# Performance work log

Measured on AMD Instinct MI355X. Metric: run time of the kernel, lower is better.

Reference implementation:

```python
import jax, jax.numpy as jnp
import numpy as np
from jax.scipy.linalg import expm

DIM = 1024
N_ROT = 3


def setup_inputs() -> dict:
    key = jax.random.key(0)
    k1, k2 = jax.random.split(key)
    x = jax.random.normal(k1, (4, 4096, DIM), dtype=jnp.float32)
    # raw parameter tensors; skew-symmetrization (as in reset_parameters) done in reference
    generators = jax.random.normal(k2, (N_ROT, DIM, DIM), dtype=jnp.float32) * 0.02
    return {"x": x, "generators": generators}


def reference(x, generators):
    # skew-symmetrize each generator: G <- 0.5*(G - G^T)
    gens = 0.5 * (generators - jnp.swapaxes(generators, -1, -2))
    # sequential rotations: x = x @ expm(G_i) for each of the N_ROT generators
    for i in range(N_ROT):
        rot = expm(gens[i])  # [DIM, DIM] orthogonal rotation
        x = x @ rot
    return x
```

## Files before the change

kernel.cpp:

```cpp
#include <hip/hip_runtime.h>

#define S 1048576
typedef unsigned short u16;
typedef unsigned int u32;
typedef __attribute__((ext_vector_type(8))) short s8v;
typedef __attribute__((ext_vector_type(4))) float f4v;

__device__ __forceinline__ float bf2f(u16 u){
    union { float f; u32 u; } v; v.u = ((u32)u) << 16; return v.f;
}
__device__ __forceinline__ u16 f2bf(float x){
    u32 u = __float_as_uint(x);
    u32 r = (u + 0x7FFFu + ((u >> 16) & 1u)) >> 16;
    return (u16)r;
}
__device__ __forceinline__ void splitf(float x, u16& h, u16& l){
    h = f2bf(x);
    l = f2bf(x - bf2f(h));
}
__device__ __forceinline__ float pairf(const u16* H, const u16* L, size_t off){
    return bf2f(H[off]) + bf2f(L[off]);
}
__device__ __forceinline__ int sidx(int r, int c){ return (r<<6) + (((c) ^ (r&7))<<3); }
__device__ __forceinline__ void gl16(const void* g, void* l){
    __builtin_amdgcn_global_load_lds((const __attribute__((address_space(1))) void*)g,
                                     (__attribute__((address_space(3))) void*)l, 16, 0, 0);
}

__global__ __launch_bounds__(256) void pre_k(const float* __restrict__ G, u16* __restrict__ Abase){
    __shared__ float Gt[64][65];
    const int bid = blockIdx.x;
    const int t = threadIdx.x;
    const int bx = bid & 15, by = (bid >> 4) & 15, z = bid >> 8;
    const float* Gz = G + (size_t)z*S;
    u16* Ah = Abase + (size_t)z*2*S;
    u16* Al = Ah + S;
    const int row = t >> 2, cq = (t & 3) << 4;
    const int r0 = by << 6, c0 = bx << 6;
    #pragma unroll
    for (int g = 0; g < 4; ++g){
        float4 v = *(const float4*)(Gz + (size_t)(c0+row)*1024 + r0 + cq + g*4);
        Gt[row][cq+g*4+0]=v.x; Gt[row][cq+g*4+1]=v.y; Gt[row][cq+g*4+2]=v.z; Gt[row][cq+g*4+3]=v.w;
    }
    __syncthreads();
    #pragma unroll
    for (int g = 0; g < 2; ++g){
        const float* p = Gz + (size_t)(r0+row)*1024 + c0 + cq + g*8;
        float4 v0 = *(const float4*)(p);
        float4 v1 = *(const float4*)(p+4);
        float xs[8] = {v0.x,v0.y,v0.z,v0.w,v1.x,v1.y,v1.z,v1.w};
        s8v sh, sl;
        #pragma unroll
        for (int i = 0; i < 8; ++i){
            float gt = Gt[cq + g*8 + i][row];
            u16 h,l; splitf(0.5f*(xs[i]-gt), h, l);
            sh[i] = (short)h; sl[i] = (short)l;
        }
        *(s8v*)(Ah + (size_t)(r0+row)*1024 + c0 + cq + g*8) = sh;
        *(s8v*)(Al + (size_t)(r0+row)*1024 + c0 + cq + g*8) = sl;
    }
}

template<int MODE>
__global__ __launch_bounds__(256) void gemm64_k(const u16* __restrict__ Abase, const u16* __restrict__ Btbase,
                                                u16* __restrict__ Cbase,
                                                const u16* __restrict__ Pab, const u16* __restrict__ Pa2b,
                                                u16* __restrict__ O2base, u16* __restrict__ E2t){
    __shared__ u16 lds[3*8192];
    const int t = threadIdx.x;
    const int z = blockIdx.z;
    const int lin = (int)blockIdx.x + ((int)blockIdx.y << 4);
    const int sw = (lin & 7)*32 + (lin >> 3);
    const int bx = sw & 15, by = sw >> 4;
    const u16* Ah = Abase  + (size_t)z*2*S;
    const u16* Bh = Btbase + (size_t)z*2*S; const u16* Bl = Bh + S;
    u16* Ch = Cbase + (size_t)z*2*S;
    const u16* Pah = Pab + (size_t)z*2*S;   const u16* Pal = Pah + S;
    const u16* P2h = Pa2b + (size_t)z*2*S;
    u16* O2h = O2base + (size_t)z*2*S;
    const int brow = by << 6, bcol = bx << 6;
    const int lane = t & 63, w = t >> 6;
    const int wm = (w >> 1) << 5, wn = (w & 1) << 5;
    const int lr = lane & 15, g = lane >> 4;
    int qq[2]; size_t goA[2], goB[2];
    #pragma unroll
    for (int i = 0; i < 2; ++i){
        int q = (((w<<1)+i)<<6) + lane;
        int r = q >> 3, c = lane & 7;
        qq[i] = q << 3;
        goA[i] = (size_t)(brow+r)*1024 + ((c^(r&7))<<3);
        goB[i] = (size_t)(bcol+r)*1024 + ((c^(r&7))<<3);
    }
    auto issue = [&](int kt){
        u16* L = lds + (kt % 3) * 8192;
        const int k0 = kt << 6;
        #pragma unroll
        for (int i = 0; i < 2; ++i){
            gl16(Ah + goA[i] + k0, L + qq[i]);
            gl16(Bh + goB[i] + k0, L + 4096 + qq[i]);
        }
    };
    issue(0); issue(1);
    f4v acc[2][2] = {};
    for (int kt = 0; kt < 16; ++kt){
        if (kt < 15) asm volatile("s_waitcnt vmcnt(4)" ::: "memory");
        else         asm volatile("s_waitcnt vmcnt(0)" ::: "memory");
        __builtin_amdgcn_s_barrier();
        __builtin_amdgcn_sched_barrier(0);
        if (kt < 14) issue(kt + 2);
        const u16* L = lds + (kt % 3) * 8192;
        #pragma unroll
        for (int ks = 0; ks < 2; ++ks){
            const int ch = (ks << 2) + g;
            s8v a_h[2], b_h[2];
            #pragma unroll
            for (int f = 0; f < 2; ++f){
                const int ra = wm+(f<<4)+lr, rb = wn+(f<<4)+lr;
                a_h[f] = *(const s8v*)&L[sidx(ra,ch)];
                b_h[f] = *(const s8v*)&L[4096 + sidx(rb,ch)];
            }
            __builtin_amdgcn_s_setprio(1);
            #pragma unroll
            for (int mf = 0; mf < 2; ++mf)
                #pragma unroll
                for (int nf = 0; nf < 2; ++nf)
                    acc[mf][nf] = __builtin_amdgcn_mfma_f32_16x16x32_bf16(a_h[mf], b_h[nf], acc[mf][nf], 0,0,0);
            __builtin_amdgcn_s_setprio(0);
        }
    }
    const int orr = g << 2;
    u16 hsv[2][2][4];
    #pragma unroll
    for (int mf = 0; mf < 2; ++mf)
        #pragma unroll
        for (int nf = 0; nf < 2; ++nf)
            #pragma unroll
            for (int r = 0; r < 4; ++r){
                const int orow = brow + wm + (mf<<4) + orr + r;
                const int ocol = bcol + wn + (nf<<4) + lr;
                const size_t off = (size_t)orow*1024 + ocol;
                const float av = acc[mf][nf][r];
                if (MODE == 0){
                    Ch[off] = f2bf(av);
                }
                if (MODE == 1){
                    Ch[off] = f2bf(av);
                    float a = pairf(Bh, Bl, off);
                    O2h[off] = f2bf((1.0f/6.0f)*a - (1.0f/24.0f)*av);
                }
                if (MODE == 2){
                    float a  = pairf(Pah, Pal, off);
                    float a2 = bf2f(P2h[off]);
                    float e = a - 0.5f*a2 - av + (orow == ocol ? 1.0f : 0.0f);
                    u16 h = f2bf(e);
                    O2h[off] = h;
                    hsv[mf][nf][r] = h;
                }
            }
    if (MODE == 2 && z == 2){
        u16 (*Tt)[72] = (u16(*)[72])lds;
        __builtin_amdgcn_s_barrier();
        #pragma unroll
        for (int mf = 0; mf < 2; ++mf)
            #pragma unroll
            for (int nf = 0; nf < 2; ++nf)
                #pragma unroll
                for (int r = 0; r < 4; ++r){
                    const int lrow = wm + (mf<<4) + orr + r;
                    const int lcol = wn + (nf<<4) + lr;
                    Tt[lcol][lrow] = hsv[mf][nf][r];
                }
        __builtin_amdgcn_s_barrier();
        const int rr = t >> 2, cc = (t & 3) << 1;
        #pragma unroll
        for (int i = 0; i < 2; ++i){
            s8v v = *(const s8v*)&Tt[rr][(cc+i)<<3];
            *(s8v*)&E2t[(size_t)(bcol+rr)*1024 + brow + ((cc+i)<<3)] = v;
        }
    }
}

__global__ __launch_bounds__(512) void gemm_big3x(const float* __restrict__ X, const u16* __restrict__ Rth,
                                                  float* __restrict__ Y){
    __shared__ u16 lds[2*32768];
    const int bid = blockIdx.x;
    const int swz = (bid & 7)*32 + (bid >> 3);
    const int by = swz >> 2, bx = swz & 3;
    const int brow = by << 8, bcol = bx << 8;
    const int t = threadIdx.x;
    const int lane = t & 63, w = t >> 6;
    const int wm = (w >> 2) << 7, wn = (w & 3) << 6;
    const int lr = lane & 15, g = lane >> 4;
    int bq[4]; size_t gb[4];
    #pragma unroll
    for (int i = 0; i < 4; ++i){
        int q = (((w<<2)+i)<<6) + lane;
        int r = q >> 3, c = lane & 7;
        bq[i] = q << 3;
        gb[i] = (size_t)(bcol+r)*1024 + ((c^(r&7))<<3);
    }
    int xrow[4], xc[4];
    #pragma unroll
    for (int i = 0; i < 4; ++i){ int q = (i<<9) + t; xrow[i] = q >> 3; xc[i] = q & 7; }
    auto issueB = [&](int kt){
        u16* L = lds + ((kt & 1) << 15) + 16384;
        const int k0 = kt << 6;
        #pragma unroll
        for (int i = 0; i < 4; ++i) gl16(Rth + gb[i] + k0, L + bq[i]);
    };
    float4 xf[4][2];
    auto loadX = [&](int kt){
        const int k0 = kt << 6;
        #pragma unroll
        for (int i = 0; i < 4; ++i){
            const float* p = X + (size_t)(brow+xrow[i])*1024 + k0 + (xc[i]<<3);
            xf[i][0] = *(const float4*)(p);
            xf[i][1] = *(const float4*)(p+4);
        }
    };
    auto writeX = [&](int kt){
        u16* L = lds + ((kt & 1) << 15);
        #pragma unroll
        for (int i = 0; i < 4; ++i){
            float xs[8] = {xf[i][0].x, xf[i][0].y, xf[i][0].z, xf[i][0].w,
                           xf[i][1].x, xf[i][1].y, xf[i][1].z, xf[i][1].w};
            s8v h;
            #pragma unroll
            for (int j = 0; j < 8; ++j) h[j] = (short)f2bf(xs[j]);
            *(s8v*)&L[sidx(xrow[i], xc[i])] = h;
        }
    };
    f4v acc[8][4] = {};
    loadX(0); issueB(0); writeX(0);
    for (int kt = 0; kt < 16; ++kt){
        __syncthreads();
        if (kt < 15){ loadX(kt + 1); issueB(kt + 1); }
        const u16* L = lds + ((kt & 1) << 15);
        #pragma unroll
        for (int ks = 0; ks < 2; ++ks){
            const int ch = (ks << 2) + g;
            s8v bh[4];
            #pragma unroll
            for (int nf = 0; nf < 4; ++nf){
                const int rb = wn+(nf<<4)+lr;
                bh[nf] = *(const s8v*)&L[16384 + sidx(rb,ch)];
            }
            __builtin_amdgcn_s_setprio(1);
            #pragma unroll
            for (int mf = 0; mf < 8; ++mf){
                const int ra = wm+(mf<<4)+lr;
                s8v a = *(const s8v*)&L[sidx(ra,ch)];
                #pragma unroll
                for (int nf = 0; nf < 4; ++nf)
                    acc[mf][nf] = __builtin_amdgcn_mfma_f32_16x16x32_bf16(a, bh[nf], acc[mf][nf], 0,0,0);
            }
            __builtin_amdgcn_s_setprio(0);
        }
        if (kt < 15) writeX(kt + 1);
    }
    const int orr = g << 2;
    #pragma unroll
    for (int mf = 0; mf < 8; ++mf)
        #pragma unroll
        for (int nf = 0; nf < 4; ++nf)
            #pragma unroll
            for (int r = 0; r < 4; ++r){
                int orow = brow + wm + (mf<<4) + orr + r;
                int ocol = bcol + wn + (nf<<4) + lr;
                Y[(size_t)orow*1024 + ocol] = acc[mf][nf][r];
            }
}

extern "C" void kernel_launch(void* const* d_in, const int* in_sizes, int n_in,
                              void* d_out, int out_size, void* d_ws, size_t ws_size,
                              hipStream_t stream) {
    const float* X = (const float*)d_in[0];
    const float* G = (const float*)d_in[1];
    float* out = (float*)d_out;
    u16* ob = (u16*)d_out;
    auto slot = [&](int i){ return ob + (size_t)i*2*S; };
    u16* RT = (u16*)d_ws;

    dim3 b(256);
    pre_k<<<dim3(768), b, 0, stream>>>(G, slot(0));
    gemm64_k<1><<<dim3(16,16,3), b, 0, stream>>>(slot(0), slot(0), slot(3),
                                                 slot(0), slot(0), slot(6), slot(15));
    gemm64_k<2><<<dim3(16,16,3), b, 0, stream>>>(slot(6), slot(3), slot(14),
                                                 slot(0), slot(3), slot(9), slot(15));
    gemm64_k<0><<<dim3(16,16,1), b, 0, stream>>>(slot(15), slot(10), slot(12),
                                                 slot(0), slot(0), slot(12), slot(15));
    gemm64_k<0><<<dim3(16,16,1), b, 0, stream>>>(slot(12), slot(9), RT,
                                                 slot(0), slot(0), RT, slot(15));
    gemm_big3x<<<dim3(256), dim3(512), 0, stream>>>(X, RT, out);
}
```

Before: 106.6 us.

## Pre-convert X to bf16 inside pre_k and use an async-LDS bf16 GEMM

Adds extra blocks to the preprocessing kernel that convert the fp32 input X to bf16 in workspace, running alongside generator preprocessing. The final big GEMM then streams bf16 X directly into LDS with global_load_lds double buffering, instead of reading and converting fp32 X inside the GEMM. This halves X traffic in the main GEMM and removes in-loop conversion, at the cost of an extra pass over X (read fp32, write bf16) in the pre kernel. It falls back to the old path if the workspace is too small.

```diff
diff --git a/kernel.cpp b/kernel.cpp
--- a/kernel.cpp
+++ b/kernel.cpp
@@ -26,11 +26,26 @@
     __builtin_amdgcn_global_load_lds((const __attribute__((address_space(1))) void*)g,
                                      (__attribute__((address_space(3))) void*)l, 16, 0, 0);
 }
-
-__global__ __launch_bounds__(256) void pre_k(const float* __restrict__ G, u16* __restrict__ Abase){
+__device__ __forceinline__ void xconv1(const float* __restrict__ X, u16* __restrict__ Xh, int u, int t){
+    const size_t idx8 = (size_t)u*2048 + (size_t)t*8;
+    float4 v0 = *(const float4*)(X+idx8);
+    float4 v1 = *(const float4*)(X+idx8+4);
+    float xs[8] = {v0.x,v0.y,v0.z,v0.w,v1.x,v1.y,v1.z,v1.w};
+    s8v h;
+    #pragma unroll
+    for (int i = 0; i < 8; ++i) h[i] = (short)f2bf(xs[i]);
+    *(s8v*)(Xh+idx8) = h;
+}
+
+__global__ __launch_bounds__(256) void pre_k(const float* __restrict__ G, u16* __restrict__ Abase,
+                                             const float* __restrict__ X, u16* __restrict__ Xh){
     __shared__ float Gt[64][65];
     const int bid = blockIdx.x;
     const int t = threadIdx.x;
+    if (bid >= 768){
+        for (int u = bid - 768; u < 8192; u += 1280) xconv1(X, Xh, u, t);
+        return;
+    }
     const int bx = bid & 15, by = (bid >> 4) & 15, z = bid >> 8;
     const float* Gz = G + (size_t)z*S;
     u16* Ah = Abase + (size_t)z*2*S;
@@ -180,6 +195,83 @@
     }
 }
 
+__global__ __launch_bounds__(512) void gemm_big3(const u16* __restrict__ Xh, const u16* __restrict__ Rth,
+                                                 float* __restrict__ Y){
+    __shared__ u16 lds[2][32768];
+    const int bid = blockIdx.x;
+    const int swz = (bid & 7)*32 + (bid >> 3);
+    const int by = swz >> 2, bx = swz & 3;
+    const int brow = by << 8, bcol = bx << 8;
+    const int t = threadIdx.x;
+    const int lane = t & 63, w = t >> 6;
+    const int wm = (w >> 2) << 7, wn = (w & 3) << 6;
+    const int lr = lane & 15, g = lane >> 4;
+    int xq[4]; size_t gx[4], gb[4];
+    #pragma unroll
+    for (int i = 0; i < 4; ++i){
+        int q = (((w<<2)+i)<<6) + lane;
+        int r = q >> 3, c = lane & 7;
+        xq[i] = q << 3;
+        gx[i] = (size_t)(brow+r)*1024 + ((c^(r&7))<<3);
+        gb[i] = (size_t)(bcol+r)*1024 + ((c^(r&7))<<3);
+    }
+    f4v acc[8][4] = {};
+    {
+        u16* L = lds[0];
+        #pragma unroll
+        for (int i = 0; i < 4; ++i){
+            gl16(Xh  + gx[i], L + xq[i]);
+            gl16(Rth + gb[i], L + 16384 + xq[i]);
+        }
+    }
+    int cur = 0;
+    for (int kt = 0; kt < 16; ++kt){
+        __syncthreads();
+        if (kt < 15){
+            u16* L = lds[cur^1];
+            const int k0 = (kt+1) << 6;
+            #pragma unroll
+            for (int i = 0; i < 4; ++i){
+                gl16(Xh  + gx[i] + k0, L + xq[i]);
+                gl16(Rth + gb[i] + k0, L + 16384 + xq[i]);
+            }
+        }
+        const u16* L = lds[cur];
+        #pragma unroll
+        for (int ks = 0; ks < 2; ++ks){
+            const int ch = (ks << 2) + g;
+            s8v bh[4];
+            #pragma unroll
+            for (int nf = 0; nf < 4; ++nf){
+                const int rb = wn+(nf<<4)+lr;
+                bh[nf] = *(const s8v*)&L[16384 + sidx(rb,ch)];
+            }
+            __builtin_amdgcn_s_setprio(1);
+            #pragma unroll
+            for (int mf = 0; mf < 8; ++mf){
+                const int ra = wm+(mf<<4)+lr;
+                s8v a = *(const s8v*)&L[sidx(ra,ch)];
+                #pragma unroll
+                for (int nf = 0; nf < 4; ++nf)
+                    acc[mf][nf] = __builtin_amdgcn_mfma_f32_16x16x32_bf16(a, bh[nf], acc[mf][nf], 0,0,0);
+            }
+            __builtin_amdgcn_s_setprio(0);
+        }
+        cur ^= 1;
+    }
+    const int orr = g << 2;
+    #pragma unroll
+    for (int mf = 0; mf < 8; ++mf)
+        #pragma unroll
+        for (int nf = 0; nf < 4; ++nf)
+            #pragma unroll
+            for (int r = 0; r < 4; ++r){
+                int orow = brow + wm + (mf<<4) + orr + r;
+                int ocol = bcol + wn + (nf<<4) + lr;
+                Y[(size_t)orow*1024 + ocol] = acc[mf][nf][r];
+            }
+}
+
 __global__ __launch_bounds__(512) void gemm_big3x(const float* __restrict__ X, const u16* __restrict__ Rth,
                                                   float* __restrict__ Y){
     __shared__ u16 lds[2*32768];
@@ -280,9 +372,11 @@
     u16* ob = (u16*)d_out;
     auto slot = [&](int i){ return ob + (size_t)i*2*S; };
     u16* RT = (u16*)d_ws;
+    u16* Xh = RT + (size_t)2*S;
+    const bool ws_ok = ws_size >= (size_t)36*S;
 
     dim3 b(256);
-    pre_k<<<dim3(768), b, 0, stream>>>(G, slot(0));
+    pre_k<<<dim3(ws_ok ? 2048 : 768), b, 0, stream>>>(G, slot(0), X, Xh);
     gemm64_k<1><<<dim3(16,16,3), b, 0, stream>>>(slot(0), slot(0), slot(3),
                                                  slot(0), slot(0), slot(6), slot(15));
     gemm64_k<2><<<dim3(16,16,3), b, 0, stream>>>(slot(6), slot(3), slot(14),
@@ -291,5 +385,8 @@
                                                  slot(0), slot(0), slot(12), slot(15));
     gemm64_k<0><<<dim3(16,16,1), b, 0, stream>>>(slot(12), slot(9), RT,
                                                  slot(0), slot(0), RT, slot(15));
-    gemm_big3x<<<dim3(256), dim3(512), 0, stream>>>(X, RT, out);
-}
+    if (ws_ok)
+        gemm_big3<<<dim3(256), dim3(512), 0, stream>>>(Xh, RT, out);
+    else
+        gemm_big3x<<<dim3(256), dim3(512), 0, stream>>>(X, RT, out);
+}
```

Measured after the change: 107.9 us. No clear change (+1.1%).
